# Kernel tuning notes

Hardware: AMD Instinct MI355X
Metric: run time of the kernel (lower is better)

The kernel has to match this reference:

```python
import jax, jax.numpy as jnp
import numpy as np
import math

HIDDEN = 32
N_NODES = 4096
N_EDGES = 8192
FEAT = HIDDEN * 16
# e3nn FullyConnectedTensorProduct instruction order: loop i_in1, i_in2, i_out
PATHS = [(l1, l2, l3) for l1 in range(4) for l2 in range(4) for l3 in range(4)
         if abs(l1 - l2) <= l3 <= l1 + l2 and (l1 + l2 + l3) % 2 == 0]
WEIGHT_NUMEL = len(PATHS) * HIDDEN * HIDDEN  # 23 * 1024 = 23552
_CNT = {l3: sum(1 for p in PATHS if p[2] == l3) for l3 in range(4)}
# path_weight: irrep_normalization='component', path_normalization='element'
PATH_W = {p: math.sqrt((2 * p[2] + 1) / (_CNT[p[2]] * HIDDEN)) for p in PATHS}


def _sh(xp, x, y, z):
    # e3nn-convention real spherical harmonics l=0..3, 'component' normalization.
    # Assumes unit-norm (x,y,z). xp is np or jnp.
    s3, s5, s7, s15 = math.sqrt(3.), math.sqrt(5.), math.sqrt(7.), math.sqrt(15.)
    c58, c38 = math.sqrt(5. / 8.), math.sqrt(3. / 8.)
    comps = [
        xp.ones_like(x),
        s3 * x, s3 * y, s3 * z,
        s5 * s3 * x * z, s5 * s3 * x * y, s5 * (y * y - 0.5 * (x * x + z * z)),
        s5 * s3 * y * z, s5 * (s3 / 2.) * (z * z - x * x),
        s7 * c58 * x * (3. * z * z - x * x), s7 * s15 * x * y * z,
        s7 * c38 * x * (5. * y * y - 1.), s7 * 0.5 * y * (5. * y * y - 3.),
        s7 * c38 * z * (5. * y * y - 1.), s7 * (s15 / 2.) * y * (z * z - x * x),
        s7 * c58 * z * (z * z - 3. * x * x),
    ]
    return xp.stack(comps, axis=-1)


def _wigner_tables():
    # Real-basis unit-Frobenius invariant tensors (e3nn wigner_3j up to sign),
    # computed as Gaunt integrals of the real SH over the sphere (exact quadrature:
    # integrand degree <= 9, Gauss-Legendre x uniform phi).
    nu, nphi = 16, 32
    u, wu = np.polynomial.legendre.leggauss(nu)
    phi = np.arange(nphi) * (2.0 * np.pi / nphi)
    uu = np.repeat(u, nphi)
    ww = np.repeat(wu, nphi) * (2.0 * np.pi / nphi)
    pp = np.tile(phi, nu)
    st = np.sqrt(np.maximum(1.0 - uu * uu, 0.0))
    Y = _sh(np, st * np.cos(pp), st * np.sin(pp), uu)  # [P,16]
    tabs = {}
    for key in set(PATHS):
        l1, l2, l3 = key
        C = np.einsum('p,pi,pj,pk->ijk', ww,
                      Y[:, l1 * l1:(l1 + 1) ** 2],
                      Y[:, l2 * l2:(l2 + 1) ** 2],
                      Y[:, l3 * l3:(l3 + 1) ** 2])
        tabs[key] = (C / np.linalg.norm(C)).astype(np.float32)
    return tabs


W3J = _wigner_tables()


def setup_inputs():
    key = jax.random.key(0)
    k1, k2, k3, k4, k5 = jax.random.split(key, 5)
    return {
        'node_features': jax.random.normal(k1, (N_NODES, FEAT), jnp.float32),
        'edge_index': jax.random.randint(k2, (2, N_EDGES), 0, N_NODES),
        'edge_vectors': jax.random.normal(k3, (N_EDGES, 3), jnp.float32),
        'w_weight': jax.random.uniform(k4, (WEIGHT_NUMEL, 1), jnp.float32, -1.0, 1.0),
        'w_bias': jax.random.uniform(k5, (WEIGHT_NUMEL,), jnp.float32, -1.0, 1.0),
    }


def reference(node_features, edge_index, edge_vectors, w_weight, w_bias):
    src, dst = edge_index[0], edge_index[1]
    N = node_features.shape[0]
    E = edge_vectors.shape[0]
    lengths = jnp.maximum(jnp.linalg.norm(edge_vectors, axis=-1, keepdims=True), 1e-8)
    unit = edge_vectors / lengths
    Y = _sh(jnp, unit[:, 0], unit[:, 1], unit[:, 2])            # [E,16]
    # weight_net: Linear(1, weight_numel)
    W = lengths * w_weight[:, 0][None, :] + w_bias[None, :]     # [E,23552]
    x_src = node_features[src]                                  # [E,512] gather
    acc = [jnp.zeros((E, HIDDEN, 2 * l + 1), node_features.dtype) for l in range(4)]
    for p_idx, (l1, l2, l3) in enumerate(PATHS):
        x1 = x_src[:, HIDDEN * l1 * l1: HIDDEN * (l1 + 1) ** 2].reshape(E, HIDDEN, 2 * l1 + 1)
        y2 = Y[:, l2 * l2:(l2 + 1) ** 2]                        # [E,2l2+1]
        C = jnp.asarray(W3J[(l1, l2, l3)])                      # [2l1+1,2l2+1,2l3+1]
        wp = W[:, p_idx * HIDDEN * HIDDEN:(p_idx + 1) * HIDDEN * HIDDEN].reshape(E, HIDDEN, HIDDEN)
        tmp = jnp.einsum('eui,ej,ijk->euk', x1, y2, C)
        acc[l3] = acc[l3] + PATH_W[(l1, l2, l3)] * jnp.einsum('euk,euw->ewk', tmp, wp)
    messages = jnp.concatenate([a.reshape(E, -1) for a in acc], axis=-1)  # [E,512]
    return jax.ops.segment_sum(messages, dst, num_segments=N)
```

## Files before the change

kernel.cpp:

```cpp
#include <hip/hip_runtime.h>
#include <math.h>

#define N_PATHS 23
#define HIDDEN  32
#define N_NODES 4096
#define N_EDGES 8192
#define FEAT    512
#define BLK     128
#define ZERO_BLOCKS 256

#define WAVE_SYNC() asm volatile("s_waitcnt lgkmcnt(0)" ::: "memory")

typedef __attribute__((ext_vector_type(8)))  short bf16x8;
typedef __attribute__((ext_vector_type(16))) float f32x16;

constexpr int cL1[N_PATHS] = {0,0,0,0, 1,1,1,1,1,1, 2,2,2,2,2,2,2, 3,3,3,3,3,3};
constexpr int cL2[N_PATHS] = {0,1,2,3, 0,1,1,2,2,3, 0,1,1,2,2,3,3, 0,1,2,2,3,3};
constexpr int cCOFF[N_PATHS]= {0,1,10,35,84,93,102,147,192,297,402,427,472,577,602,727,832,1077,1126,1231,1336,1581,1630};
constexpr int cL3P[N_PATHS] = {0,5,13,21, 1,4,7,11,15,19, 2,6,9,10,14,18,22, 3,8,12,16,17,20};
constexpr int cL3S[5] = {0,4,10,17,23};
constexpr int cOFF3[4] = {0,32,128,288};
__device__ const int CNT_L3[4] = {4,6,7,6};
__device__ const int D_L3[N_PATHS] = {0,1,2,3, 1,0,2,1,3,2, 2,1,3,0,2,1,3, 3,2,1,3,0,2};

__device__ const double GLX8[8] = {
    -0.96028985649753623168, -0.79666647741362673959, -0.52553240991632898582, -0.18343464249564980494,
     0.18343464249564980494,  0.52553240991632898582,  0.79666647741362673959,  0.96028985649753623168};
__device__ const double GLW8[8] = {
     0.10122853629037625915,  0.22238103445337447054,  0.31370664587788728734,  0.36268378337836198297,
     0.36268378337836198297,  0.31370664587788728734,  0.22238103445337447054,  0.10122853629037625915};
__device__ const double COSP16[16] = {
  1.0,                     0.92387953251128675613,  0.70710678118654752440,  0.38268343236508977173,
  0.0,                    -0.38268343236508977173, -0.70710678118654752440, -0.92387953251128675613,
 -1.0,                    -0.92387953251128675613, -0.70710678118654752440, -0.38268343236508977173,
  0.0,                     0.38268343236508977173,  0.70710678118654752440,  0.92387953251128675613};
__device__ const double SINP16[16] = {
  0.0,                     0.38268343236508977173,  0.70710678118654752440,  0.92387953251128675613,
  1.0,                     0.92387953251128675613,  0.70710678118654752440,  0.38268343236508977173,
  0.0,                    -0.38268343236508977173, -0.70710678118654752440, -0.92387953251128675613,
 -1.0,                    -0.92387953251128675613, -0.70710678118654752440, -0.38268343236508977173};

__device__ inline void sh_f64(double x, double y, double z, double* Y) {
    const double s3 = 1.7320508075688772935, s5 = 2.2360679774997896964,
                 s7 = 2.6457513110645905905, s15 = 3.8729833462074168852;
    const double c58 = 0.79056941504209483300, c38 = 0.61237243569579452455;
    Y[0] = 1.0;
    Y[1] = s3*x;  Y[2] = s3*y;  Y[3] = s3*z;
    Y[4] = s5*s3*x*z;  Y[5] = s5*s3*x*y;
    Y[6] = s5*(y*y - 0.5*(x*x + z*z));
    Y[7] = s5*s3*y*z;  Y[8] = s5*(s3/2.0)*(z*z - x*x);
    Y[9] = s7*c58*x*(3.0*z*z - x*x);
    Y[10]= s7*s15*x*y*z;
    Y[11]= s7*c38*x*(5.0*y*y - 1.0);
    Y[12]= s7*0.5*y*(5.0*y*y - 3.0);
    Y[13]= s7*c38*z*(5.0*y*y - 1.0);
    Y[14]= s7*(s15/2.0)*y*(z*z - x*x);
    Y[15]= s7*c58*z*(z*z - 3.0*x*x);
}

__device__ inline void sh_f32(float x, float y, float z, float* Y) {
    const float s3 = 1.73205080757f, s5 = 2.23606797750f, s7 = 2.64575131106f, s15 = 3.87298334621f;
    const float c58 = 0.79056941504f, c38 = 0.61237243570f;
    Y[0] = 1.0f;
    Y[1] = s3*x;  Y[2] = s3*y;  Y[3] = s3*z;
    Y[4] = s15*x*z;  Y[5] = s15*x*y;
    Y[6] = s5*(y*y - 0.5f*(x*x + z*z));
    Y[7] = s15*y*z;  Y[8] = s5*(s3*0.5f)*(z*z - x*x);
    Y[9] = s7*c58*x*(3.0f*z*z - x*x);
    Y[10]= s7*s15*x*y*z;
    Y[11]= s7*c38*x*(5.0f*y*y - 1.0f);
    Y[12]= s7*0.5f*y*(5.0f*y*y - 3.0f);
    Y[13]= s7*c38*z*(5.0f*y*y - 1.0f);
    Y[14]= s7*(s15*0.5f)*y*(z*z - x*x);
    Y[15]= s7*c58*z*(z*z - 3.0f*x*x);
}

__device__ inline unsigned short bf16rne(float x) {
    unsigned int u = __float_as_uint(x);
    unsigned int r = (u + 0x7FFFu + ((u >> 16) & 1u)) >> 16;
    return (unsigned short)r;
}
__device__ inline float bf16f(unsigned short h) {
    return __uint_as_float(((unsigned int)h) << 16);
}

__global__ __launch_bounds__(512) void w3j_setup_kernel(
    const float* __restrict__ ww, const float* __restrict__ wb,
    float* __restrict__ g_w3j,
    unsigned short* __restrict__ Awhi, unsigned short* __restrict__ Awlo,
    unsigned short* __restrict__ Abhi, unsigned short* __restrict__ Ablo,
    float* __restrict__ out) {
    const int t = threadIdx.x;

    if (blockIdx.x >= N_PATHS) {
        const int b = blockIdx.x - N_PATHS;
        float4* o4 = (float4*)(out + (size_t)b * (N_NODES*FEAT/ZERO_BLOCKS));
#pragma unroll
        for (int r = 0; r < 4; ++r)
            o4[t + 512*r] = make_float4(0.f,0.f,0.f,0.f);
        return;
    }

    __shared__ float s_Yq[128][17];
    __shared__ float s_wq[128];
    __shared__ float s_part[256];
    __shared__ float red[256];
    __shared__ float s_scale;

    const int p = blockIdx.x;
    const int l1 = cL1[p], l2 = cL2[p];
    const int l3 = D_L3[p];
    const int d2 = 2*l2+1, d3 = 2*l3+1;
    const int csize = (2*l1+1)*d2*d3;
    const double step = 2.0*3.14159265358979323846/16.0;

#pragma unroll
    for (int r = 0; r < 2; ++r) {
        const int idx = t + 512*r;
        const int w = idx >> 5, u = idx & 31;
        const float vw = ww[p*1024 + u*32 + w];
        const float vb = wb[p*1024 + u*32 + w];
        const unsigned short hw = bf16rne(vw);
        const unsigned short hb = bf16rne(vb);
        const int o = p*1024 + w*32 + u;
        Awhi[o] = hw;  Awlo[o] = bf16rne(vw - bf16f(hw));
        Abhi[o] = hb;  Ablo[o] = bf16rne(vb - bf16f(hb));
    }

    if (t < 128) {
        const int iu = t >> 4, ip = t & 15;
        const double u = GLX8[iu];
        const double st = sqrt(fmax(1.0 - u*u, 0.0));
        double Y[16];
        sh_f64(st*COSP16[ip], st*SINP16[ip], u, Y);
#pragma unroll
        for (int i = 0; i < 16; ++i) s_Yq[t][i] = (float)Y[i];
        s_wq[t] = (float)(GLW8[iu] * step);
    }
    __syncthreads();

    const int entry0 = t >> 2, sub = t & 3;
#pragma unroll
    for (int pass = 0; pass < 2; ++pass) {
        const int entry = entry0 + pass*128;
        float acc = 0.f;
        if (entry < csize) {
            const int i = entry/(d2*d3); const int r = entry - i*(d2*d3);
            const int j = r/d3; const int k = r - j*d3;
            const int ai = l1*l1+i, bi = l2*l2+j, ci = l3*l3+k;
#pragma unroll 4
            for (int it = 0; it < 32; ++it) {
                const int q = it*4 + sub;
                acc = fmaf(s_wq[q] * s_Yq[q][ai] * s_Yq[q][bi], s_Yq[q][ci], acc);
            }
        }
        acc += __shfl_xor(acc, 1);
        acc += __shfl_xor(acc, 2);
        if (sub == 0 && entry < csize) s_part[entry] = acc;
    }
    __syncthreads();

    if (t < 256) { const float v = (t < csize) ? s_part[t] : 0.f; red[t] = v*v; }
    __syncthreads();
    for (int s = 128; s > 0; s >>= 1) {
        if (t < s) red[t] += red[t+s];
        __syncthreads();
    }
    if (t == 0) {
        const float pw = sqrtf((float)(2*l3+1) / ((float)CNT_L3[l3] * (float)HIDDEN));
        s_scale = pw / sqrtf(red[0]);
    }
    __syncthreads();
    if (t < csize) g_w3j[cCOFF[p] + t] = s_part[t] * s_scale;
}

template<int G, int P>
__device__ __forceinline__ void do_path(
    int lane, int el4, int u0, int bvaddr, int avaddr,
    const float (&xr0)[16], const float (&xr1)[16],
    const float* __restrict__ w3j,
    const unsigned short* __restrict__ Awhi, const unsigned short* __restrict__ Awlo,
    const unsigned short* __restrict__ Abhi, const unsigned short* __restrict__ Ablo,
    const float* sY, float* sz,
    unsigned short* sbh, unsigned short* sbl,
    f32x16 &Cw, f32x16 &Cb)
{
    constexpr int l1 = cL1[P], l2 = cL2[P];
    constexpr int d1 = 2*l1+1, d2 = 2*l2+1, d3 = 2*G+1;
    constexpr int zc = d1*d3;
    constexpr int xo = l1*l1;

#pragma unroll
    for (int base = 0; base < 4*zc; base += 64) {
        const int idx = base + lane;
        if (idx < 4*zc) {
            const int elz = idx / zc;
            const int r = idx - elz*zc;
            const int i = r / d3, k = r - i*d3;
            const float* Cp = w3j + cCOFF[P] + i*(d2*d3) + k;
            const float* Yp = sY + elz*16 + l2*l2;
            float acc = 0.f;
#pragma unroll
            for (int j = 0; j < d2; ++j) acc = fmaf(Yp[j], Cp[j*d3], acc);
            sz[elz*50 + r] = acc;
        }
    }
    WAVE_SYNC();

    const unsigned short* pwh = Awhi + P*1024;
    const unsigned short* pwl = Awlo + P*1024;
    const unsigned short* pbh = Abhi + P*1024;
    const unsigned short* pbl = Ablo + P*1024;
    bf16x8 awh[2], awl[2], abh[2], abl[2];
#pragma unroll
    for (int kc = 0; kc < 2; ++kc) {
        awh[kc] = *(const bf16x8*)(pwh + avaddr + kc*16);
        awl[kc] = *(const bf16x8*)(pwl + avaddr + kc*16);
        abh[kc] = *(const bf16x8*)(pbh + avaddr + kc*16);
        abl[kc] = *(const bf16x8*)(pbl + avaddr + kc*16);
    }

    {
        const float* zr = sz + el4*50;
        unsigned short* bh = sbh + (el4*d3)*40 + 2*u0;
        unsigned short* bl = sbl + (el4*d3)*40 + 2*u0;
#pragma unroll
        for (int k = 0; k < d3; ++k) {
            float t0 = 0.f, t1 = 0.f;
#pragma unroll
            for (int i = 0; i < d1; ++i) {
                const float zz = zr[i*d3 + k];
                t0 = fmaf(xr0[xo+i], zz, t0);
                t1 = fmaf(xr1[xo+i], zz, t1);
            }
            const unsigned int b0 = __float_as_uint(t0);
            const unsigned int b1 = __float_as_uint(t1);
            const float l0 = t0 - __uint_as_float(b0 & 0xFFFF0000u);
            const float l1f = t1 - __uint_as_float(b1 & 0xFFFF0000u);
            *(unsigned int*)(bh + k*40) = (b0 >> 16) | (b1 & 0xFFFF0000u);
            *(unsigned int*)(bl + k*40) = (__float_as_uint(l0) >> 16) | (__float_as_uint(l1f) & 0xFFFF0000u);
        }
    }
    WAVE_SYNC();

#pragma unroll
    for (int kc = 0; kc < 2; ++kc) {
        const bf16x8 bh = *(const bf16x8*)(sbh + bvaddr + kc*16);
        const bf16x8 bl = *(const bf16x8*)(sbl + bvaddr + kc*16);
        Cw = __builtin_amdgcn_mfma_f32_32x32x16_bf16(awh[kc], bh, Cw, 0, 0, 0);
        Cb = __builtin_amdgcn_mfma_f32_32x32x16_bf16(abh[kc], bh, Cb, 0, 0, 0);
        Cw = __builtin_amdgcn_mfma_f32_32x32x16_bf16(awh[kc], bl, Cw, 0, 0, 0);
        Cb = __builtin_amdgcn_mfma_f32_32x32x16_bf16(abh[kc], bl, Cb, 0, 0, 0);
        Cw = __builtin_amdgcn_mfma_f32_32x32x16_bf16(awl[kc], bh, Cw, 0, 0, 0);
        Cb = __builtin_amdgcn_mfma_f32_32x32x16_bf16(abl[kc], bh, Cb, 0, 0, 0);
    }
    WAVE_SYNC();
}

template<int G>
__device__ __forceinline__ void do_group(
    int lane, int el4, int u0, int bvaddr, int avaddr,
    const float (&xr0)[16], const float (&xr1)[16],
    const float* __restrict__ w3j,
    const unsigned short* __restrict__ Awhi, const unsigned short* __restrict__ Awlo,
    const unsigned short* __restrict__ Abhi, const unsigned short* __restrict__ Ablo,
    const float* sY, float* sz,
    unsigned short* sbh, unsigned short* sbl,
    const float* slen, float* smsg)
{
    constexpr int d3 = 2*G+1;
    constexpr int s = cL3S[G];
    constexpr int n = cL3S[G+1] - cL3S[G];
    f32x16 Cw = (f32x16)(0.f), Cb = (f32x16)(0.f);

    do_path<G, cL3P[s+0]>(lane,el4,u0,bvaddr,avaddr,xr0,xr1,w3j,Awhi,Awlo,Abhi,Ablo,sY,sz,sbh,sbl,Cw,Cb);
    do_path<G, cL3P[s+1]>(lane,el4,u0,bvaddr,avaddr,xr0,xr1,w3j,Awhi,Awlo,Abhi,Ablo,sY,sz,sbh,sbl,Cw,Cb);
    do_path<G, cL3P[s+2]>(lane,el4,u0,bvaddr,avaddr,xr0,xr1,w3j,Awhi,Awlo,Abhi,Ablo,sY,sz,sbh,sbl,Cw,Cb);
    do_path<G, cL3P[s+3]>(lane,el4,u0,bvaddr,avaddr,xr0,xr1,w3j,Awhi,Awlo,Abhi,Ablo,sY,sz,sbh,sbl,Cw,Cb);
    if constexpr (n > 4)
        do_path<G, cL3P[s+4]>(lane,el4,u0,bvaddr,avaddr,xr0,xr1,w3j,Awhi,Awlo,Abhi,Ablo,sY,sz,sbh,sbl,Cw,Cb);
    if constexpr (n > 5)
        do_path<G, cL3P[s+5]>(lane,el4,u0,bvaddr,avaddr,xr0,xr1,w3j,Awhi,Awlo,Abhi,Ablo,sY,sz,sbh,sbl,Cw,Cb);
    if constexpr (n > 6)
        do_path<G, cL3P[s+6]>(lane,el4,u0,bvaddr,avaddr,xr0,xr1,w3j,Awhi,Awlo,Abhi,Ablo,sY,sz,sbh,sbl,Cw,Cb);

    const int col = lane & 31;
    if (col < 4*d3) {
        const int elc = col / d3, k = col - elc*d3;
        const float len = slen[elc];
        float* mp = smsg + elc*FEAT + cOFF3[G] + k;
#pragma unroll
        for (int reg = 0; reg < 16; ++reg) {
            const int w = (reg & 3) + 8*(reg >> 2) + 4*(lane >> 5);
            mp[w*d3] = fmaf(len, Cw[reg], Cb[reg]);
        }
    }
}

__global__ __launch_bounds__(BLK) void edge_kernel(
    const float* __restrict__ nf,
    const int*   __restrict__ eidx,
    const float* __restrict__ ev,
    const float* __restrict__ w3j,
    const unsigned short* __restrict__ Awhi,
    const unsigned short* __restrict__ Awlo,
    const unsigned short* __restrict__ Abhi,
    const unsigned short* __restrict__ Ablo,
    float*       __restrict__ out)
{
    __shared__ float s_zp[2][200];
    __shared__ float s_Y[2][64];
    __shared__ float s_len[2][4];
    __shared__ int   s_src[2][4];
    __shared__ int   s_dst[2][4];
    __shared__ __align__(16) unsigned short s_Bhi[2][1280];
    __shared__ __align__(16) unsigned short s_Blo[2][1280];
    __shared__ float s_msg[2][4*FEAT];

    const int t    = threadIdx.x;
    const int wave = t >> 6;
    const int lane = t & 63;
    const int el4  = lane >> 4;
    const int u0   = lane & 15;
    const int e0   = blockIdx.x * 8 + wave*4;
    const int bvaddr = (lane & 31)*40 + (lane >> 5)*8;
    const int avaddr = (lane & 31)*32 + (lane >> 5)*8;

    if (lane < 4) {
        const int e = e0 + lane;
        s_src[wave][lane] = eidx[e];
        s_dst[wave][lane] = eidx[N_EDGES + e];
        const float x = ev[e*3+0], y = ev[e*3+1], z = ev[e*3+2];
        const float len = sqrtf(x*x + y*y + z*z);
        const float lc = fmaxf(len, 1e-8f);
        s_len[wave][lane] = lc;
        float Yl[16];
        sh_f32(x/lc, y/lc, z/lc, Yl);
#pragma unroll
        for (int i = 0; i < 16; ++i) s_Y[wave][lane*16+i] = Yl[i];
    }
    WAVE_SYNC();

    float xr0[16], xr1[16];
    {
        const float* xrow = nf + (size_t)s_src[wave][el4]*FEAT;
        const int ua = 2*u0, ub = 2*u0 + 1;
        xr0[0] = xrow[ua];                 xr1[0] = xrow[ub];
#pragma unroll
        for (int i = 0; i < 3; ++i) { xr0[1+i] = xrow[32 + ua*3 + i];  xr1[1+i] = xrow[32 + ub*3 + i]; }
#pragma unroll
        for (int i = 0; i < 5; ++i) { xr0[4+i] = xrow[128 + ua*5 + i]; xr1[4+i] = xrow[128 + ub*5 + i]; }
#pragma unroll
        for (int i = 0; i < 7; ++i) { xr0[9+i] = xrow[288 + ua*7 + i]; xr1[9+i] = xrow[288 + ub*7 + i]; }
    }

    do_group<0>(lane,el4,u0,bvaddr,avaddr,xr0,xr1,w3j,Awhi,Awlo,Abhi,Ablo,
                s_Y[wave], s_zp[wave], s_Bhi[wave], s_Blo[wave], s_len[wave], s_msg[wave]);
    do_group<1>(lane,el4,u0,bvaddr,avaddr,xr0,xr1,w3j,Awhi,Awlo,Abhi,Ablo,
                s_Y[wave], s_zp[wave], s_Bhi[wave], s_Blo[wave], s_len[wave], s_msg[wave]);
    do_group<2>(lane,el4,u0,bvaddr,avaddr,xr0,xr1,w3j,Awhi,Awlo,Abhi,Ablo,
                s_Y[wave], s_zp[wave], s_Bhi[wave], s_Blo[wave], s_len[wave], s_msg[wave]);
    do_group<3>(lane,el4,u0,bvaddr,avaddr,xr0,xr1,w3j,Awhi,Awlo,Abhi,Ablo,
                s_Y[wave], s_zp[wave], s_Bhi[wave], s_Blo[wave], s_len[wave], s_msg[wave]);
    WAVE_SYNC();

    for (int i = lane; i < 4*FEAT; i += 64) {
        const int elc = i >> 9, m = i & 511;
        atomicAdd(&out[(size_t)s_dst[wave][elc]*FEAT + m], s_msg[wave][i]);
    }
}

extern "C" void kernel_launch(void* const* d_in, const int* in_sizes, int n_in,
                              void* d_out, int out_size, void* d_ws, size_t ws_size,
                              hipStream_t stream) {
    const float* nf   = (const float*)d_in[0];
    const int*   eidx = (const int*)  d_in[1];
    const float* ev   = (const float*)d_in[2];
    const float* ww   = (const float*)d_in[3];
    const float* wb   = (const float*)d_in[4];
    float* out = (float*)d_out;

    float* w3j = (float*)d_ws;
    unsigned short* Awhi = (unsigned short*)((char*)d_ws + 16384);
    unsigned short* Awlo = Awhi + N_PATHS*1024;
    unsigned short* Abhi = Awlo + N_PATHS*1024;
    unsigned short* Ablo = Abhi + N_PATHS*1024;

    w3j_setup_kernel<<<N_PATHS + ZERO_BLOCKS, 512, 0, stream>>>(
        ww, wb, w3j, Awhi, Awlo, Abhi, Ablo, out);
    edge_kernel<<<N_EDGES/8, BLK, 0, stream>>>(nf, eidx, ev, w3j, Awhi, Awlo, Abhi, Ablo, out);
}
```

Before: 121.4 us.

## Process eight edges per wave, reusing A-weight fragments across two MFMA tiles

Each wave now handles eight edges instead of four. The per-path weight fragments (A operands) loaded from global memory are reused across two 32-column B tiles, which halves weight loads per edge. Blocks shrink to a single wave of 64 threads, so each lane holds four channels of node features. This raises register pressure (4x16 feature registers and four accumulators) and reduces waves per block, which could lower occupancy or latency hiding.

```diff
diff --git a/kernel.cpp b/kernel.cpp
--- a/kernel.cpp
+++ b/kernel.cpp
@@ -6,7 +6,7 @@
 #define N_NODES 4096
 #define N_EDGES 8192
 #define FEAT    512
-#define BLK     128
+#define BLK     64
 #define ZERO_BLOCKS 256
 
 #define WAVE_SYNC() asm volatile("s_waitcnt lgkmcnt(0)" ::: "memory")
@@ -176,14 +176,14 @@
 
 template<int G, int P>
 __device__ __forceinline__ void do_path(
-    int lane, int el4, int u0, int bvaddr, int avaddr,
-    const float (&xr0)[16], const float (&xr1)[16],
+    int lane, int el8, int u3, int bvoff, int avaddr,
+    const float (&xr)[4][16],
     const float* __restrict__ w3j,
     const unsigned short* __restrict__ Awhi, const unsigned short* __restrict__ Awlo,
     const unsigned short* __restrict__ Abhi, const unsigned short* __restrict__ Ablo,
     const float* sY, float* sz,
-    unsigned short* sbh, unsigned short* sbl,
-    f32x16 &Cw, f32x16 &Cb)
+    unsigned short (*sbh)[1280], unsigned short (*sbl)[1280],
+    f32x16 (&Cw)[2], f32x16 (&Cb)[2])
 {
     constexpr int l1 = cL1[P], l2 = cL2[P];
     constexpr int d1 = 2*l1+1, d2 = 2*l2+1, d3 = 2*G+1;
@@ -191,9 +191,9 @@
     constexpr int xo = l1*l1;
 
 #pragma unroll
-    for (int base = 0; base < 4*zc; base += 64) {
+    for (int base = 0; base < 8*zc; base += 64) {
         const int idx = base + lane;
-        if (idx < 4*zc) {
+        if (idx < 8*zc) {
             const int elz = idx / zc;
             const int r = idx - elz*zc;
             const int i = r / d3, k = r - i*d3;
@@ -202,7 +202,7 @@
             float acc = 0.f;
 #pragma unroll
             for (int j = 0; j < d2; ++j) acc = fmaf(Yp[j], Cp[j*d3], acc);
-            sz[elz*50 + r] = acc;
+            sz[idx] = acc;
         }
     }
     WAVE_SYNC();
@@ -221,78 +221,106 @@
     }
 
     {
-        const float* zr = sz + el4*50;
-        unsigned short* bh = sbh + (el4*d3)*40 + 2*u0;
-        unsigned short* bl = sbl + (el4*d3)*40 + 2*u0;
+        const float* zr = sz + el8*zc;
+        const int tile = el8 >> 2, elL = el8 & 3;
+        unsigned short* bh = sbh[tile] + (elL*d3)*40 + 4*u3;
+        unsigned short* bl = sbl[tile] + (elL*d3)*40 + 4*u3;
 #pragma unroll
         for (int k = 0; k < d3; ++k) {
-            float t0 = 0.f, t1 = 0.f;
+            float tv[4] = {0.f, 0.f, 0.f, 0.f};
 #pragma unroll
             for (int i = 0; i < d1; ++i) {
                 const float zz = zr[i*d3 + k];
-                t0 = fmaf(xr0[xo+i], zz, t0);
-                t1 = fmaf(xr1[xo+i], zz, t1);
+#pragma unroll
+                for (int r = 0; r < 4; ++r) tv[r] = fmaf(xr[r][xo+i], zz, tv[r]);
             }
-            const unsigned int b0 = __float_as_uint(t0);
-            const unsigned int b1 = __float_as_uint(t1);
-            const float l0 = t0 - __uint_as_float(b0 & 0xFFFF0000u);
-            const float l1f = t1 - __uint_as_float(b1 & 0xFFFF0000u);
-            *(unsigned int*)(bh + k*40) = (b0 >> 16) | (b1 & 0xFFFF0000u);
-            *(unsigned int*)(bl + k*40) = (__float_as_uint(l0) >> 16) | (__float_as_uint(l1f) & 0xFFFF0000u);
+            unsigned int hi01, hi23, lo01, lo23;
+            {
+                const unsigned int b0 = __float_as_uint(tv[0]);
+                const unsigned int b1 = __float_as_uint(tv[1]);
+                const unsigned int b2 = __float_as_uint(tv[2]);
+                const unsigned int b3 = __float_as_uint(tv[3]);
+                const float l0 = tv[0] - __uint_as_float(b0 & 0xFFFF0000u);
+                const float l1f = tv[1] - __uint_as_float(b1 & 0xFFFF0000u);
+                const float l2f = tv[2] - __uint_as_float(b2 & 0xFFFF0000u);
+                const float l3f = tv[3] - __uint_as_float(b3 & 0xFFFF0000u);
+                hi01 = (b0 >> 16) | (b1 & 0xFFFF0000u);
+                hi23 = (b2 >> 16) | (b3 & 0xFFFF0000u);
+                lo01 = (__float_as_uint(l0) >> 16) | (__float_as_uint(l1f) & 0xFFFF0000u);
+                lo23 = (__float_as_uint(l2f) >> 16) | (__float_as_uint(l3f) & 0xFFFF0000u);
+            }
+            *(unsigned int*)(bh + k*40)     = hi01;
+            *(unsigned int*)(bh + k*40 + 2) = hi23;
+            *(unsigned int*)(bl + k*40)     = lo01;
+            *(unsigned int*)(bl + k*40 + 2) = lo23;
         }
     }
     WAVE_SYNC();
 
 #pragma unroll
     for (int kc = 0; kc < 2; ++kc) {
-        const bf16x8 bh = *(const bf16x8*)(sbh + bvaddr + kc*16);
-        const bf16x8 bl = *(const bf16x8*)(sbl + bvaddr + kc*16);
-        Cw = __builtin_amdgcn_mfma_f32_32x32x16_bf16(awh[kc], bh, Cw, 0, 0, 0);
-        Cb = __builtin_amdgcn_mfma_f32_32x32x16_bf16(abh[kc], bh, Cb, 0, 0, 0);
-        Cw = __builtin_amdgcn_mfma_f32_32x32x16_bf16(awh[kc], bl, Cw, 0, 0, 0);
-        Cb = __builtin_amdgcn_mfma_f32_32x32x16_bf16(abh[kc], bl, Cb, 0, 0, 0);
-        Cw = __builtin_amdgcn_mfma_f32_32x32x16_bf16(awl[kc], bh, Cw, 0, 0, 0);
-        Cb = __builtin_amdgcn_mfma_f32_32x32x16_bf16(abl[kc], bh, Cb, 0, 0, 0);
+        const bf16x8 bh0 = *(const bf16x8*)(sbh[0] + bvoff + kc*16);
+        const bf16x8 bl0 = *(const bf16x8*)(sbl[0] + bvoff + kc*16);
+        const bf16x8 bh1 = *(const bf16x8*)(sbh[1] + bvoff + kc*16);
+        const bf16x8 bl1 = *(const bf16x8*)(sbl[1] + bvoff + kc*16);
+        Cw[0] = __builtin_amdgcn_mfma_f32_32x32x16_bf16(awh[kc], bh0, Cw[0], 0, 0, 0);
+        Cw[1] = __builtin_amdgcn_mfma_f32_32x32x16_bf16(awh[kc], bh1, Cw[1], 0, 0, 0);
+        Cb[0] = __builtin_amdgcn_mfma_f32_32x32x16_bf16(abh[kc], bh0, Cb[0], 0, 0, 0);
+        Cb[1] = __builtin_amdgcn_mfma_f32_32x32x16_bf16(abh[kc], bh1, Cb[1], 0, 0, 0);
+        Cw[0] = __builtin_amdgcn_mfma_f32_32x32x16_bf16(awh[kc], bl0, Cw[0], 0, 0, 0);
+        Cw[1] = __builtin_amdgcn_mfma_f32_32x32x16_bf16(awh[kc], bl1, Cw[1], 0, 0, 0);
+        Cb[0] = __builtin_amdgcn_mfma_f32_32x32x16_bf16(abh[kc], bl0, Cb[0], 0, 0, 0);
+        Cb[1] = __builtin_amdgcn_mfma_f32_32x32x16_bf16(abh[kc], bl1, Cb[1], 0, 0, 0);
+        Cw[0] = __builtin_amdgcn_mfma_f32_32x32x16_bf16(awl[kc], bh0, Cw[0], 0, 0, 0);
+        Cw[1] = __builtin_amdgcn_mfma_f32_32x32x16_bf16(awl[kc], bh1, Cw[1], 0, 0, 0);
+        Cb[0] = __builtin_amdgcn_mfma_f32_32x32x16_bf16(abl[kc], bh0, Cb[0], 0, 0, 0);
+        Cb[1] = __builtin_amdgcn_mfma_f32_32x32x16_bf16(abl[kc], bh1, Cb[1], 0, 0, 0);
     }
     WAVE_SYNC();
 }
 
 template<int G>
 __device__ __forceinline__ void do_group(
-    int lane, int el4, int u0, int bvaddr, int avaddr,
-    const float (&xr0)[16], const float (&xr1)[16],
+    int lane, int el8, int u3, int bvoff, int avaddr,
+    const float (&xr)[4][16],
     const float* __restrict__ w3j,
     const unsigned short* __restrict__ Awhi, const unsigned short* __restrict__ Awlo,
     const unsigned short* __restrict__ Abhi, const unsigned short* __restrict__ Ablo,
     const float* sY, float* sz,
-    unsigned short* sbh, unsigned short* sbl,
+    unsigned short (*sbh)[1280], unsigned short (*sbl)[1280],
     const float* slen, float* smsg)
 {
     constexpr int d3 = 2*G+1;
     constexpr int s = cL3S[G];
     constexpr int n = cL3S[G+1] - cL3S[G];
-    f32x16 Cw = (f32x16)(0.f), Cb = (f32x16)(0.f);
-
-    do_path<G, cL3P[s+0]>(lane,el4,u0,bvaddr,avaddr,xr0,xr1,w3j,Awhi,Awlo,Abhi,Ablo,sY,sz,sbh,sbl,Cw,Cb);
-    do_path<G, cL3P[s+1]>(lane,el4,u0,bvaddr,avaddr,xr0,xr1,w3j,Awhi,Awlo,Abhi,Ablo,sY,sz,sbh,sbl,Cw,Cb);
-    do_path<G, cL3P[s+2]>(lane,el4,u0,bvaddr,avaddr,xr0,xr1,w3j,Awhi,Awlo,Abhi,Ablo,sY,sz,sbh,sbl,Cw,Cb);
-    do_path<G, cL3P[s+3]>(lane,el4,u0,bvaddr,avaddr,xr0,xr1,w3j,Awhi,Awlo,Abhi,Ablo,sY,sz,sbh,sbl,Cw,Cb);
+    f32x16 Cw[2], Cb[2];
+    Cw[0] = (f32x16)(0.f); Cw[1] = (f32x16)(0.f);
+    Cb[0] = (f32x16)(0.f); Cb[1] = (f32x16)(0.f);
+
+    do_path<G, cL3P[s+0]>(lane,el8,u3,bvoff,avaddr,xr,w3j,Awhi,Awlo,Abhi,Ablo,sY,sz,sbh,sbl,Cw,Cb);
+    do_path<G, cL3P[s+1]>(lane,el8,u3,bvoff,avaddr,xr,w3j,Awhi,Awlo,Abhi,Ablo,sY,sz,sbh,sbl,Cw,Cb);
+    do_path<G, cL3P[s+2]>(lane,el8,u3,bvoff,avaddr,xr,w3j,Awhi,Awlo,Abhi,Ablo,sY,sz,sbh,sbl,Cw,Cb);
+    do_path<G, cL3P[s+3]>(lane,el8,u3,bvoff,avaddr,xr,w3j,Awhi,Awlo,Abhi,Ablo,sY,sz,sbh,sbl,Cw,Cb);
     if constexpr (n > 4)
-        do_path<G, cL3P[s+4]>(lane,el4,u0,bvaddr,avaddr,xr0,xr1,w3j,Awhi,Awlo,Abhi,Ablo,sY,sz,sbh,sbl,Cw,Cb);
+        do_path<G, cL3P[s+4]>(lane,el8,u3,bvoff,avaddr,xr,w3j,Awhi,Awlo,Abhi,Ablo,sY,sz,sbh,sbl,Cw,Cb);
     if constexpr (n > 5)
-        do_path<G, cL3P[s+5]>(lane,el4,u0,bvaddr,avaddr,xr0,xr1,w3j,Awhi,Awlo,Abhi,Ablo,sY,sz,sbh,sbl,Cw,Cb);
+        do_path<G, cL3P[s+5]>(lane,el8,u3,bvoff,avaddr,xr,w3j,Awhi,Awlo,Abhi,Ablo,sY,sz,sbh,sbl,Cw,Cb);
     if constexpr (n > 6)
-        do_path<G, cL3P[s+6]>(lane,el4,u0,bvaddr,avaddr,xr0,xr1,w3j,Awhi,Awlo,Abhi,Ablo,sY,sz,sbh,sbl,Cw,Cb);
+        do_path<G, cL3P[s+6]>(lane,el8,u3,bvoff,avaddr,xr,w3j,Awhi,Awlo,Abhi,Ablo,sY,sz,sbh,sbl,Cw,Cb);
 
     const int col = lane & 31;
     if (col < 4*d3) {
-        const int elc = col / d3, k = col - elc*d3;
-        const float len = slen[elc];
-        float* mp = smsg + elc*FEAT + cOFF3[G] + k;
-#pragma unroll
-        for (int reg = 0; reg < 16; ++reg) {
-            const int w = (reg & 3) + 8*(reg >> 2) + 4*(lane >> 5);
-            mp[w*d3] = fmaf(len, Cw[reg], Cb[reg]);
+        const int elcL = col / d3, k = col - elcL*d3;
+#pragma unroll
+        for (int tile = 0; tile < 2; ++tile) {
+            const int elc = tile*4 + elcL;
+            const float len = slen[elc];
+            float* mp = smsg + elc*FEAT + cOFF3[G] + k;
+#pragma unroll
+            for (int reg = 0; reg < 16; ++reg) {
+                const int w = (reg & 3) + 8*(reg >> 2) + 4*(lane >> 5);
+                mp[w*d3] = fmaf(len, Cw[tile][reg], Cb[tile][reg]);
+            }
         }
     }
 }
@@ -308,65 +336,66 @@
     const unsigned short* __restrict__ Ablo,
     float*       __restrict__ out)
 {
-    __shared__ float s_zp[2][200];
-    __shared__ float s_Y[2][64];
-    __shared__ float s_len[2][4];
-    __shared__ int   s_src[2][4];
-    __shared__ int   s_dst[2][4];
+    __shared__ float s_zp[8*49];
+    __shared__ float s_Y[8*16];
+    __shared__ float s_len[8];
+    __shared__ int   s_src[8];
+    __shared__ int   s_dst[8];
     __shared__ __align__(16) unsigned short s_Bhi[2][1280];
     __shared__ __align__(16) unsigned short s_Blo[2][1280];
-    __shared__ float s_msg[2][4*FEAT];
-
-    const int t    = threadIdx.x;
-    const int wave = t >> 6;
-    const int lane = t & 63;
-    const int el4  = lane >> 4;
-    const int u0   = lane & 15;
-    const int e0   = blockIdx.x * 8 + wave*4;
-    const int bvaddr = (lane & 31)*40 + (lane >> 5)*8;
+    __shared__ float s_msg[8*FEAT];
+
+    const int lane = threadIdx.x;
+    const int el8  = lane >> 3;
+    const int u3   = lane & 7;
+    const int e0   = blockIdx.x * 8;
+    const int bvoff  = (lane & 31)*40 + (lane >> 5)*8;
     const int avaddr = (lane & 31)*32 + (lane >> 5)*8;
 
-    if (lane < 4) {
+    if (lane < 8) {
         const int e = e0 + lane;
-        s_src[wave][lane] = eidx[e];
-        s_dst[wave][lane] = eidx[N_EDGES + e];
+        s_src[lane] = eidx[e];
+        s_dst[lane] = eidx[N_EDGES + e];
         const float x = ev[e*3+0], y = ev[e*3+1], z = ev[e*3+2];
         const float len = sqrtf(x*x + y*y + z*z);
         const float lc = fmaxf(len, 1e-8f);
-        s_len[wave][lane] = lc;
+        s_len[lane] = lc;
         float Yl[16];
         sh_f32(x/lc, y/lc, z/lc, Yl);
 #pragma unroll
-        for (int i = 0; i < 16; ++i) s_Y[wave][lane*16+i] = Yl[i];
+        for (int i = 0; i < 16; ++i) s_Y[lane*16+i] = Yl[i];
     }
     WAVE_SYNC();
 
-    float xr0[16], xr1[16];
+    float xr[4][16];
     {
-        const float* xrow = nf + (size_t)s_src[wave][el4]*FEAT;
-        const int ua = 2*u0, ub = 2*u0 + 1;
-        xr0[0] = xrow[ua];                 xr1[0] = xrow[ub];
-#pragma unroll
-        for (int i = 0; i < 3; ++i) { xr0[1+i] = xrow[32 + ua*3 + i];  xr1[1+i] = xrow[32 + ub*3 + i]; }
-#pragma unroll
-        for (int i = 0; i < 5; ++i) { xr0[4+i] = xrow[128 + ua*5 + i]; xr1[4+i] = xrow[128 + ub*5 + i]; }
-#pragma unroll
-        for (int i = 0; i < 7; ++i) { xr0[9+i] = xrow[288 + ua*7 + i]; xr1[9+i] = xrow[288 + ub*7 + i]; }
-    }
-
-    do_group<0>(lane,el4,u0,bvaddr,avaddr,xr0,xr1,w3j,Awhi,Awlo,Abhi,Ablo,
-                s_Y[wave], s_zp[wave], s_Bhi[wave], s_Blo[wave], s_len[wave], s_msg[wave]);
-    do_group<1>(lane,el4,u0,bvaddr,avaddr,xr0,xr1,w3j,Awhi,Awlo,Abhi,Ablo,
-                s_Y[wave], s_zp[wave], s_Bhi[wave], s_Blo[wave], s_len[wave], s_msg[wave]);
-    do_group<2>(lane,el4,u0,bvaddr,avaddr,xr0,xr1,w3j,Awhi,Awlo,Abhi,Ablo,
-                s_Y[wave], s_zp[wave], s_Bhi[wave], s_Blo[wave], s_len[wave], s_msg[wave]);
-    do_group<3>(lane,el4,u0,bvaddr,avaddr,xr0,xr1,w3j,Awhi,Awlo,Abhi,Ablo,
-                s_Y[wave], s_zp[wave], s_Bhi[wave], s_Blo[wave], s_len[wave], s_msg[wave]);
+        const float* xrow = nf + (size_t)s_src[el8]*FEAT;
+#pragma unroll
+        for (int r = 0; r < 4; ++r) {
+            const int u = 4*u3 + r;
+            xr[r][0] = xrow[u];
+#pragma unroll
+            for (int i = 0; i < 3; ++i) xr[r][1+i] = xrow[32 + u*3 + i];
+#pragma unroll
+            for (int i = 0; i < 5; ++i) xr[r][4+i] = xrow[128 + u*5 + i];
+#pragma unroll
+            for (int i = 0; i < 7; ++i) xr[r][9+i] = xrow[288 + u*7 + i];
+        }
+    }
+
+    do_group<0>(lane,el8,u3,bvoff,avaddr,xr,w3j,Awhi,Awlo,Abhi,Ablo,
+                s_Y, s_zp, s_Bhi, s_Blo, s_len, s_msg);
+    do_group<1>(lane,el8,u3,bvoff,avaddr,xr,w3j,Awhi,Awlo,Abhi,Ablo,
+                s_Y, s_zp, s_Bhi, s_Blo, s_len, s_msg);
+    do_group<2>(lane,el8,u3,bvoff,avaddr,xr,w3j,Awhi,Awlo,Abhi,Ablo,
+                s_Y, s_zp, s_Bhi, s_Blo, s_len, s_msg);
+    do_group<3>(lane,el8,u3,bvoff,avaddr,xr,w3j,Awhi,Awlo,Abhi,Ablo,
+                s_Y, s_zp, s_Bhi, s_Blo, s_len, s_msg);
     WAVE_SYNC();
 
-    for (int i = lane; i < 4*FEAT; i += 64) {
+    for (int i = lane; i < 8*FEAT; i += 64) {
         const int elc = i >> 9, m = i & 511;
-        atomicAdd(&out[(size_t)s_dst[wave][elc]*FEAT + m], s_msg[wave][i]);
+        atomicAdd(&out[(size_t)s_dst[elc]*FEAT + m], s_msg[i]);
     }
 }
 
```

New measurement: 123.1 us. Within noise of the previous version (+1.4%).
